# Optimization experiments

Measured on AMD Instinct MI355X. Metric: run time of the kernel, lower is better.

Reference implementation:

```python
import jax, jax.numpy as jnp
import numpy as np

B, N, HID = 2, 1024, 2048
H, KVH, D = 16, 4, 128
GROUPS = H // KVH
FLA_W = 0.5
GATE_NORM = 16.0  # gate_logit_normalizer in source


def setup_inputs() -> dict:
    key = jax.random.key(0)
    ks = jax.random.split(key, 5)
    s = 0.02
    return {
        "hidden_states": jax.random.normal(ks[0], (B, N, HID), jnp.float32),
        "Wq": jax.random.normal(ks[1], (HID, H * D), jnp.float32) * s,
        "Wk": jax.random.normal(ks[2], (HID, KVH * D), jnp.float32) * s,
        "Wv": jax.random.normal(ks[3], (HID, KVH * D), jnp.float32) * s,
        "Wo": jax.random.normal(ks[4], (H * D, HID), jnp.float32) * s,
    }


def _heads(x, h):
    # (B, N, h*D) -> (B, h, N, D)
    return x.reshape(B, N, h, D).transpose(0, 2, 1, 3)


def _repeat_kv(x):
    # (B, KVH, N, D) -> (B, H, N, D), each kv head repeated GROUPS times
    return jnp.repeat(x, GROUPS, axis=1)


def _delta_rule(q, k, v, beta):
    # q,k,v,beta: (L, D). Token-level delta-rule recurrence, mathematically
    # identical to the chunked algorithm for any chunk_size.
    # S_t = S_{t-1} + k_t (beta_t * (v_t - S_{t-1}^T k_t))^T ;  o_t = S_t^T q_t
    Dk = q.shape[-1]
    Dv = v.shape[-1]

    def step(S, inp):
        qi, ki, vi, bi = inp
        u = bi * (vi - ki @ S)          # (Dv,)
        S = S + jnp.outer(ki, u)        # (Dk, Dv)
        return S, qi @ S                # o_t

    S0 = jnp.zeros((Dk, Dv), q.dtype)
    _, o = jax.lax.scan(step, S0, (q, k, v, beta))
    return o


def reference(hidden_states, Wq, Wk, Wv, Wo):
    q = hidden_states @ Wq              # (B, N, H*D)
    k = hidden_states @ Wk              # (B, N, KVH*D)
    v = hidden_states @ Wv              # (B, N, KVH*D)
    g = k  # AdaptiveAvgPool1d(output=KVH*D) over a length-(KVH*D) axis == identity

    qh = _heads(q, H)                   # (B, H, N, D)
    kh = _repeat_kv(_heads(k, KVH))     # (B, H, N, D)
    vh = _repeat_kv(_heads(v, KVH))
    gh = _repeat_kv(_heads(g, KVH))

    # --- linear (delta-rule) branch ---
    ql = jax.nn.softmax(qh, axis=-1)
    kl = jax.nn.softmax(kh, axis=-1)
    gl = jax.nn.log_sigmoid(gh) / GATE_NORM
    # faithful to source: flatten (B,H,N,D) -> (B*H*N, D), single recurrence
    o_lin = _delta_rule(
        ql.reshape(-1, D), kl.reshape(-1, D),
        vh.reshape(-1, D), gl.reshape(-1, D),
    )
    o_lin = o_lin.reshape(B, H, N, D).transpose(0, 2, 1, 3).reshape(B, N, H * D)
    o_lin = o_lin @ Wo                  # (B, N, HID)

    # --- base attention branch (causal GQA softmax attention) ---
    scale = 1.0 / np.sqrt(D).astype(np.float32)
    scores = jnp.einsum('bhnd,bhmd->bhnm', qh, kh) * scale  # (B,H,N,N)
    causal = jnp.tril(jnp.ones((N, N), bool))
    scores = jnp.where(causal, scores, jnp.finfo(scores.dtype).min)
    attn = jax.nn.softmax(scores, axis=-1)
    o_base = jnp.einsum('bhnm,bhmd->bhnd', attn, vh)
    o_base = o_base.transpose(0, 2, 1, 3).reshape(B, N, H * D) @ Wo

    out = FLA_W * o_lin + (1.0 - FLA_W) * o_base
    return out
```

## Files before the change

kernel.cpp:

```cpp
#include <hip/hip_runtime.h>
#include <hip/hip_bf16.h>
#include <hip/hip_fp16.h>
#include <math.h>

#define BB 2
#define NN 1024
#define HID 2048
#define NH 16
#define KVH 4
#define DD 128
#define L_TOTAL 32768
#define TOK 2048
#define NCHUNK 512

typedef __bf16 bf16;
typedef __bf16 bf16x8 __attribute__((ext_vector_type(8)));
typedef __bf16 bf16x4 __attribute__((ext_vector_type(4)));
typedef float f32x4 __attribute__((ext_vector_type(4)));

template<bool SPLIT, bool OUTBF>
__global__ __launch_bounds__(256)
void gemm_bt(const bf16* __restrict__ A, const bf16* __restrict__ Alo,
             const bf16* __restrict__ B, const bf16* __restrict__ Blo,
             float* __restrict__ Cf, bf16* __restrict__ Cb,
             int M, int N, int K, int lda, int ldb, int ldc,
             long aSb, long aSh, long aSz, long bSb, long bSh, long cSz,
             int zH, int gShift, int z0)
{
    const int zc   = blockIdx.z;
    const int z    = zc + z0;
    const int b    = z / zH;
    const int h    = z % zH;
    const int lane = threadIdx.x & 63;
    const int wave = threadIdx.x >> 6;
    const int tiles_n = N >> 4;
    const int tile = blockIdx.x * 4 + wave;
    const int mt   = tile / tiles_n;
    const int nt   = tile % tiles_n;

    const long aoff = (long)b * aSb + (long)h * aSh + (long)zc * aSz;
    const long boff = (long)b * bSb + (long)(h >> gShift) * bSh;

    const bf16* ap = A + aoff + (long)(mt * 16 + (lane & 15)) * lda + ((lane >> 4) << 3);
    const bf16* bp = B + boff + (long)(nt * 16 + (lane & 15)) * ldb + ((lane >> 4) << 3);

    f32x4 acc = {0.f, 0.f, 0.f, 0.f};
    if (!SPLIT) {
        for (int k0 = 0; k0 < K; k0 += 32) {
            bf16x8 av = *(const bf16x8*)ap;
            bf16x8 bv = *(const bf16x8*)bp;
            acc = __builtin_amdgcn_mfma_f32_16x16x32_bf16(av, bv, acc, 0, 0, 0);
            ap += 32; bp += 32;
        }
    } else {
        const bf16* apl = Alo + (ap - A);
        const bf16* bpl = Blo + (bp - B);
        for (int k0 = 0; k0 < K; k0 += 32) {
            bf16x8 av = *(const bf16x8*)ap;
            bf16x8 bv = *(const bf16x8*)bp;
            bf16x8 al = *(const bf16x8*)apl;
            bf16x8 bl = *(const bf16x8*)bpl;
            acc = __builtin_amdgcn_mfma_f32_16x16x32_bf16(av, bv, acc, 0, 0, 0);
            acc = __builtin_amdgcn_mfma_f32_16x16x32_bf16(al, bv, acc, 0, 0, 0);
            acc = __builtin_amdgcn_mfma_f32_16x16x32_bf16(av, bl, acc, 0, 0, 0);
            ap += 32; bp += 32; apl += 32; bpl += 32;
        }
    }

    const long cbase = (long)zc * cSz + (long)(nt * 16 + (lane & 15));
    const int  r0    = mt * 16 + ((lane >> 4) << 2);
    #pragma unroll
    for (int r = 0; r < 4; ++r) {
        long idx = cbase + (long)(r0 + r) * ldc;
        if (OUTBF) Cb[idx] = (bf16)acc[r];
        else       Cf[idx] = acc[r];
    }
}

__global__ void cast_split_k(const float* __restrict__ in, bf16* __restrict__ hi,
                             bf16* __restrict__ lo, long n)
{
    long i = (long)blockIdx.x * blockDim.x + threadIdx.x;
    if (i < n) {
        float x = in[i];
        bf16 h = (bf16)x;
        hi[i] = h;
        lo[i] = (bf16)(x - (float)h);
    }
}

__global__ void cast_k(const float* __restrict__ in, bf16* __restrict__ out, long n)
{
    long i = (long)blockIdx.x * blockDim.x + threadIdx.x;
    if (i < n) out[i] = (bf16)in[i];
}

__global__ void transpose_split_k(const float* __restrict__ in, bf16* __restrict__ hi,
                                  bf16* __restrict__ lo, int K, int N)
{
    long i = (long)blockIdx.x * blockDim.x + threadIdx.x;
    if (i < (long)K * N) {
        int n = (int)(i / K);
        int k = (int)(i % K);
        float x = in[(long)k * N + n];
        bf16 h = (bf16)x;
        hi[i] = h;
        lo[i] = (bf16)(x - (float)h);
    }
}

__global__ void vtrans_k(const float* __restrict__ v, bf16* __restrict__ vT)
{
    long i = (long)blockIdx.x * blockDim.x + threadIdx.x;
    if (i < 1048576) {
        int m   = (int)(i & 1023);
        int d   = (int)((i >> 10) & 127);
        int kvh = (int)((i >> 17) & 3);
        int b   = (int)(i >> 19);
        vT[i] = (bf16)v[((long)(b * 1024 + m)) * 512 + kvh * 128 + d];
    }
}

__global__ void softmax128_k(const float* __restrict__ in, float* __restrict__ out)
{
    const int row  = blockIdx.x;
    const int lane = threadIdx.x;
    float2 v = ((const float2*)(in + (long)row * 128))[lane];
    float m = fmaxf(v.x, v.y);
    #pragma unroll
    for (int s = 1; s < 64; s <<= 1) m = fmaxf(m, __shfl_xor(m, s, 64));
    float ex = expf(v.x - m), ey = expf(v.y - m);
    float sum = ex + ey;
    #pragma unroll
    for (int s = 1; s < 64; s <<= 1) sum += __shfl_xor(sum, s, 64);
    float inv = 1.0f / sum;
    ((float2*)(out + (long)row * 128))[lane] = make_float2(ex * inv, ey * inv);
}

__global__ void logsig_k(const float* __restrict__ in, float* __restrict__ out, long n)
{
    long i = (long)blockIdx.x * blockDim.x + threadIdx.x;
    if (i < n) {
        float x = in[i];
        float l = log1pf(expf(-fabsf(x)));
        out[i] = (fminf(x, 0.f) - l) * 0.0625f;
    }
}

__global__ void softmax_causal_k(bf16* __restrict__ P)
{
    const int row  = blockIdx.x;
    const int qi   = row & 1023;
    const int lane = threadIdx.x;
    bf16* p = P + (long)row * 1024;
    const float scale = 0.08838834764831845f;
    float vals[16];
    float m = -3.0e38f;
    #pragma unroll
    for (int t = 0; t < 16; ++t) {
        int j = lane + t * 64;
        float x = (j <= qi) ? (float)p[j] * scale : -3.0e38f;
        vals[t] = x;
        m = fmaxf(m, x);
    }
    #pragma unroll
    for (int s = 1; s < 64; s <<= 1) m = fmaxf(m, __shfl_xor(m, s, 64));
    float sum = 0.f;
    #pragma unroll
    for (int t = 0; t < 16; ++t) {
        float e = (vals[t] > -1.0e38f) ? expf(vals[t] - m) : 0.f;
        vals[t] = e;
        sum += e;
    }
    #pragma unroll
    for (int s = 1; s < 64; s <<= 1) sum += __shfl_xor(sum, s, 64);
    float inv = 1.f / sum;
    #pragma unroll
    for (int t = 0; t < 16; ++t) {
        int j = lane + t * 64;
        p[j] = (bf16)(vals[t] * inv);
    }
}

__global__ void ktrans_k(const float* __restrict__ KLb, bf16* __restrict__ KThi,
                         bf16* __restrict__ KTlo)
{
    long i = (long)blockIdx.x * blockDim.x + threadIdx.x;
    if (i < 1048576) {
        int t = (int)(i & 63);
        int d = (int)((i >> 6) & 127);
        int a = (int)(i >> 13);
        int b = a >> 6, kvh = (a >> 4) & 3, nc = a & 15;
        float x = KLb[((long)(b * 1024 + nc * 64 + t)) * 512 + kvh * 128 + d];
        bf16 h = (bf16)x;
        KThi[i] = h;
        KTlo[i] = (bf16)(x - (float)h);
    }
}

__global__ __launch_bounds__(256)
void prepA_mfma_k(const bf16* __restrict__ KLhi, const bf16* __restrict__ KLlo,
                  bf16* __restrict__ Abhi, bf16* __restrict__ Ablo,
                  float* __restrict__ ATf)
{
    const int a = blockIdx.x;
    const int b = a >> 6, kvh = (a >> 4) & 3, nc = a & 15;
    const long rbase = ((long)(b * 1024 + nc * 64)) * 512 + kvh * 128;
    const int wave = threadIdx.x >> 6, lane = threadIdx.x & 63;
    const int l15 = lane & 15, kq = lane >> 4;

    #pragma unroll
    for (int it = 0; it < 4; ++it) {
        const int tile = wave * 4 + it;
        const int mt = tile >> 2, nt = tile & 3;
        f32x4 acc = {0.f, 0.f, 0.f, 0.f};
        if (nt <= mt) {
            const long arow = rbase + (long)(mt * 16 + l15) * 512 + kq * 8;
            const long brow = rbase + (long)(nt * 16 + l15) * 512 + kq * 8;
            #pragma unroll
            for (int ki = 0; ki < 4; ++ki) {
                bf16x8 ah = *(const bf16x8*)(KLhi + arow + ki * 32);
                bf16x8 al = *(const bf16x8*)(KLlo + arow + ki * 32);
                bf16x8 bh = *(const bf16x8*)(KLhi + brow + ki * 32);
                bf16x8 bl = *(const bf16x8*)(KLlo + brow + ki * 32);
                acc = __builtin_amdgcn_mfma_f32_16x16x32_bf16(ah, bh, acc, 0, 0, 0);
                acc = __builtin_amdgcn_mfma_f32_16x16x32_bf16(al, bh, acc, 0, 0, 0);
                acc = __builtin_amdgcn_mfma_f32_16x16x32_bf16(ah, bl, acc, 0, 0, 0);
            }
        }
        const int s  = nt * 16 + l15;
        const int r0 = mt * 16 + kq * 4;
        #pragma unroll
        for (int r = 0; r < 4; ++r) {
            int t = r0 + r;
            float dot = (s < t) ? acc[r] : 0.f;
            bf16 hh = (bf16)dot;
            Abhi[(long)a * 4096 + t * 64 + s] = hh;
            Ablo[(long)a * 4096 + t * 64 + s] = (bf16)(dot - (float)hh);
            ATf[(long)a * 4096 + s * 64 + t] = dot;
        }
    }
}

__global__ __launch_bounds__(256)
void prepAq_mfma_k(const bf16* __restrict__ QLhi, const bf16* __restrict__ QLlo,
                   const bf16* __restrict__ KLhi, const bf16* __restrict__ KLlo,
                   bf16* __restrict__ Aqhi, bf16* __restrict__ Aqlo)
{
    const int c = blockIdx.x;
    const int b = c >> 8, h = (c >> 4) & 15, nc = c & 15, kvh = h >> 2;
    const long qb = ((long)(b * 1024 + nc * 64)) * 2048 + h * 128;
    const long kb = ((long)(b * 1024 + nc * 64)) * 512 + kvh * 128;
    const int wave = threadIdx.x >> 6, lane = threadIdx.x & 63;
    const int l15 = lane & 15, kq = lane >> 4;

    #pragma unroll
    for (int it = 0; it < 4; ++it) {
        const int tile = wave * 4 + it;
        const int mt = tile >> 2, nt = tile & 3;
        f32x4 acc = {0.f, 0.f, 0.f, 0.f};
        if (nt <= mt) {
            const long arow = qb + (long)(mt * 16 + l15) * 2048 + kq * 8;
            const long brow = kb + (long)(nt * 16 + l15) * 512 + kq * 8;
            #pragma unroll
            for (int ki = 0; ki < 4; ++ki) {
                bf16x8 ah = *(const bf16x8*)(QLhi + arow + ki * 32);
                bf16x8 al = *(const bf16x8*)(QLlo + arow + ki * 32);
                bf16x8 bh = *(const bf16x8*)(KLhi + brow + ki * 32);
                bf16x8 bl = *(const bf16x8*)(KLlo + brow + ki * 32);
                acc = __builtin_amdgcn_mfma_f32_16x16x32_bf16(ah, bh, acc, 0, 0, 0);
                acc = __builtin_amdgcn_mfma_f32_16x16x32_bf16(al, bh, acc, 0, 0, 0);
                acc = __builtin_amdgcn_mfma_f32_16x16x32_bf16(ah, bl, acc, 0, 0, 0);
            }
        }
        const int s  = nt * 16 + l15;
        const int r0 = mt * 16 + kq * 4;
        #pragma unroll
        for (int r = 0; r < 4; ++r) {
            int t = r0 + r;
            float dot = (s <= t) ? acc[r] : 0.f;
            bf16 hh = (bf16)dot;
            Aqhi[(long)c * 4096 + t * 64 + s] = hh;
            Aqlo[(long)c * 4096 + t * 64 + s] = (bf16)(dot - (float)hh);
        }
    }
}

__global__ __launch_bounds__(64, 1)
void seq_scan_k(const bf16* __restrict__ KLhi, const bf16* __restrict__ KLlo,
                const bf16* __restrict__ KThi, const bf16* __restrict__ KTlo,
                const bf16* __restrict__ Abhi, const bf16* __restrict__ Ablo,
                const float* __restrict__ ATf, const float* __restrict__ vf,
                const float* __restrict__ GLb,
                bf16* __restrict__ S0Thi, bf16* __restrict__ S0Tlo,
                bf16* __restrict__ uTghi, bf16* __restrict__ uTglo)
{
    __shared__ __align__(16) bf16  SThi[16 * 128];
    __shared__ __align__(16) bf16  STlo[16 * 128];
    __shared__ __align__(16) bf16  uThi[16 * 64];
    __shared__ __align__(16) bf16  uTlo[16 * 64];
    __shared__ __align__(16) float xb[64 * 16];
    __shared__ __align__(16) float ATl[4096];

    const int lane  = threadIdx.x;
    const int jloc  = lane & 15;
    const int kq    = lane >> 4;
    const int jglob = blockIdx.x * 16 + jloc;

    for (int i = lane; i < 16 * 128; i += 64) { SThi[i] = (bf16)0.f; STlo[i] = (bf16)0.f; }
    for (int i = lane; i < 16 * 128; i += 64) {
        int j = i >> 7, d = i & 127;
        long off = (long)(blockIdx.x * 16 + j) * 128 + d;
        S0Thi[off] = (bf16)0.f;
        S0Tlo[off] = (bf16)0.f;
    }

    f32x4 S[8];
    #pragma unroll
    for (int m = 0; m < 8; ++m) S[m] = (f32x4){0.f, 0.f, 0.f, 0.f};

    for (int c = 0; c < NCHUNK; ++c) {
        const int b = c >> 8, h = (c >> 4) & 15, nc = c & 15;
        const int kvh = h >> 2, n0 = nc * 64;
        const long krow0  = ((long)(b * 1024 + n0)) * 512 + kvh * 128;
        const int  achunk = (b * 4 + kvh) * 16 + nc;
        const long abase  = (long)achunk * 4096;
        const long ktbase = (long)achunk * 8192;

        bf16x8 klh[16], kll[16];
        #pragma unroll
        for (int m = 0; m < 4; ++m)
            #pragma unroll
            for (int ki = 0; ki < 4; ++ki) {
                long ko = krow0 + (long)(m * 16 + jloc) * 512 + ki * 32 + kq * 8;
                klh[m * 4 + ki] = *(const bf16x8*)(KLhi + ko);
                kll[m * 4 + ki] = *(const bf16x8*)(KLlo + ko);
            }

        float4 atReg[16];
        {
            const float* src = ATf + abase;
            #pragma unroll
            for (int u = 0; u < 16; ++u)
                atReg[u] = *(const float4*)(src + u * 256 + lane * 4);
        }

        bf16x8 abh[4], abl[4];
        #pragma unroll
        for (int q = 0; q < 4; ++q) {
            const int tt = (q < 2) ? (16 + q * 16) : 48;
            const int kk = (q == 3) ? 1 : 0;
            long ao = abase + (long)(tt + jloc) * 64 + kk * 32 + kq * 8;
            abh[q] = *(const bf16x8*)(Abhi + ao);
            abl[q] = *(const bf16x8*)(Ablo + ao);
        }

        float Vv[2][16], Bv[2][16];
        {
            const long vrow0 = ((long)(b * 1024 + n0)) * 512 + kvh * 128 + jglob;
            #pragma unroll
            for (int s = 0; s < 16; ++s) {
                Vv[0][s] = vf[vrow0 + (long)s * 512];
                Bv[0][s] = GLb[vrow0 + (long)s * 512];
            }
        }

        f32x4 W[4];
        #pragma unroll
        for (int m = 0; m < 4; ++m) W[m] = (f32x4){0.f, 0.f, 0.f, 0.f};
        #pragma unroll
        for (int ki = 0; ki < 4; ++ki) {
            bf16x8 sh = *(const bf16x8*)&SThi[jloc * 128 + ki * 32 + kq * 8];
            bf16x8 sl = *(const bf16x8*)&STlo[jloc * 128 + ki * 32 + kq * 8];
            #pragma unroll
            for (int m = 0; m < 4; ++m) {
                W[m] = __builtin_amdgcn_mfma_f32_16x16x32_bf16(klh[m * 4 + ki], sh, W[m], 0, 0, 0);
                W[m] = __builtin_amdgcn_mfma_f32_16x16x32_bf16(kll[m * 4 + ki], sh, W[m], 0, 0, 0);
                W[m] = __builtin_amdgcn_mfma_f32_16x16x32_bf16(klh[m * 4 + ki], sl, W[m], 0, 0, 0);
            }
        }
        #pragma unroll
        for (int m = 0; m < 4; ++m)
            #pragma unroll
            for (int r = 0; r < 4; ++r)
                xb[(m * 16 + kq * 4 + r) * 16 + jloc] = W[m][r];

        #pragma unroll
        for (int u = 0; u < 16; ++u)
            *(float4*)(ATl + u * 256 + lane * 4) = atReg[u];

        bf16x8 kth[16], ktl[16];
        #pragma unroll
        for (int m = 0; m < 8; ++m)
            #pragma unroll
            for (int ki = 0; ki < 2; ++ki) {
                long o = ktbase + (long)(m * 16 + jloc) * 64 + ki * 32 + kq * 8;
                kth[m * 2 + ki] = *(const bf16x8*)(KThi + o);
                ktl[m * 2 + ki] = *(const bf16x8*)(KTlo + o);
            }

        {
            uint4 z = {0u, 0u, 0u, 0u};
            ((uint4*)uThi)[lane] = z; ((uint4*)uThi)[lane + 64] = z;
            ((uint4*)uTlo)[lane] = z; ((uint4*)uTlo)[lane + 64] = z;
        }

        #pragma unroll
        for (int i = 0; i < 4; ++i) {
            const int T0 = i * 16;
            if (i > 0) {
                const int K32 = (i + 1) >> 1;
                const int fb  = i - 1;
                f32x4 corr = (f32x4){0.f, 0.f, 0.f, 0.f};
                #pragma unroll
                for (int ki = 0; ki < 2; ++ki) if (ki < K32) {
                    bf16x8 uh = *(const bf16x8*)&uThi[jloc * 64 + ki * 32 + kq * 8];
                    bf16x8 ul = *(const bf16x8*)&uTlo[jloc * 64 + ki * 32 + kq * 8];
                    corr = __builtin_amdgcn_mfma_f32_16x16x32_bf16(uh, abh[fb + ki], corr, 0, 0, 0);
                    corr = __builtin_amdgcn_mfma_f32_16x16x32_bf16(ul, abh[fb + ki], corr, 0, 0, 0);
                    corr = __builtin_amdgcn_mfma_f32_16x16x32_bf16(uh, abl[fb + ki], corr, 0, 0, 0);
                }
                #pragma unroll
                for (int r = 0; r < 4; ++r)
                    xb[(T0 + jloc) * 16 + kq * 4 + r] += corr[r];
            }

            float Xv[16];
            #pragma unroll
            for (int s = 0; s < 16; ++s) Xv[s] = xb[(T0 + s) * 16 + jloc];

            if (i < 3) {
                const long vrow0n = ((long)(b * 1024 + n0 + T0 + 16)) * 512 + kvh * 128 + jglob;
                #pragma unroll
                for (int s = 0; s < 16; ++s) {
                    Vv[(i + 1) & 1][s] = vf[vrow0n + (long)s * 512];
                    Bv[(i + 1) & 1][s] = GLb[vrow0n + (long)s * 512];
                }
            }

            float rb[4][16];
            #pragma unroll
            for (int p = 0; p < 4; ++p) {
                const float* rp = ATl + (T0 + p) * 64 + T0;
                #pragma unroll
                for (int g = 0; g < 4; ++g) {
                    float4 v4 = *(const float4*)(rp + g * 4);
                    rb[p][g * 4 + 0] = v4.x; rb[p][g * 4 + 1] = v4.y;
                    rb[p][g * 4 + 2] = v4.z; rb[p][g * 4 + 3] = v4.w;
                }
            }

            float acc[16];
            #pragma unroll
            for (int t = 0; t < 16; ++t) acc[t] = 0.f;

            #pragma unroll
            for (int s = 0; s < 16; ++s) {
                float u = Bv[i & 1][s] * (Vv[i & 1][s] - Xv[s] - acc[s]);
                bf16 uh = (bf16)u;
                bf16 ul = (bf16)(u - (float)uh);
                if (lane < 16) {
                    uThi[jloc * 64 + T0 + s] = uh;
                    uTlo[jloc * 64 + T0 + s] = ul;
                }
                #pragma unroll
                for (int t = 0; t < 16; ++t)
                    if (t > s) acc[t] += rb[s & 3][t] * u;
                {
                    int rr = T0 + s + 4; if (rr > 63) rr = 63;
                    const float* rp = ATl + rr * 64 + T0;
                    #pragma unroll
                    for (int g = 0; g < 4; ++g) {
                        float4 v4 = *(const float4*)(rp + g * 4);
                        rb[s & 3][g * 4 + 0] = v4.x; rb[s & 3][g * 4 + 1] = v4.y;
                        rb[s & 3][g * 4 + 2] = v4.z; rb[s & 3][g * 4 + 3] = v4.w;
                    }
                }
            }
        }

        #pragma unroll
        for (int ki = 0; ki < 2; ++ki) {
            bf16x8 uh = *(const bf16x8*)&uThi[jloc * 64 + ki * 32 + kq * 8];
            bf16x8 ul = *(const bf16x8*)&uTlo[jloc * 64 + ki * 32 + kq * 8];
            #pragma unroll
            for (int m = 0; m < 8; ++m) {
                S[m] = __builtin_amdgcn_mfma_f32_16x16x32_bf16(kth[m * 2 + ki], uh, S[m], 0, 0, 0);
                S[m] = __builtin_amdgcn_mfma_f32_16x16x32_bf16(kth[m * 2 + ki], ul, S[m], 0, 0, 0);
                S[m] = __builtin_amdgcn_mfma_f32_16x16x32_bf16(ktl[m * 2 + ki], uh, S[m], 0, 0, 0);
            }
        }

        {
            const uint4* uh4 = (const uint4*)uThi;
            const uint4* ul4 = (const uint4*)uTlo;
            uint4* gh = (uint4*)(uTghi + ((long)c * 128 + blockIdx.x * 16) * 64);
            uint4* gl = (uint4*)(uTglo + ((long)c * 128 + blockIdx.x * 16) * 64);
            gh[lane] = uh4[lane]; gh[lane + 64] = uh4[lane + 64];
            gl[lane] = ul4[lane]; gl[lane + 64] = ul4[lane + 64];
        }

        #pragma unroll
        for (int m = 0; m < 8; ++m) {
            bf16x4 h4, l4;
            #pragma unroll
            for (int r = 0; r < 4; ++r) {
                float v = S[m][r];
                bf16 hh = (bf16)v;
                h4[r] = hh;
                l4[r] = (bf16)(v - (float)hh);
            }
            int d0 = m * 16 + kq * 4;
            *(bf16x4*)&SThi[jloc * 128 + d0] = h4;
            *(bf16x4*)&STlo[jloc * 128 + d0] = l4;
            long goff = (long)(c + 1) * 16384 + (long)jglob * 128 + d0;
            *(bf16x4*)(S0Thi + goff) = h4;
            *(bf16x4*)(S0Tlo + goff) = l4;
        }
    }
}

__global__ __launch_bounds__(256)
void pass2_o_k(const bf16* __restrict__ QLhi, const bf16* __restrict__ QLlo,
               const bf16* __restrict__ S0Thi, const bf16* __restrict__ S0Tlo,
               const bf16* __restrict__ Aqhi, const bf16* __restrict__ Aqlo,
               const bf16* __restrict__ uTghi, const bf16* __restrict__ uTglo,
               float* __restrict__ O)
{
    const int c    = blockIdx.x >> 3;
    const int tg   = blockIdx.x & 7;
    const int wave = threadIdx.x >> 6;
    const int lane = threadIdx.x & 63;
    const int tt   = tg * 4 + wave;
    const int mt   = tt >> 3, nt = tt & 7;
    const int b = c >> 8, h = (c >> 4) & 15, nc = c & 15, n0 = nc * 64;
    const int kq = lane >> 4, l15 = lane & 15;

    const long qrow   = ((long)(b * 1024 + n0 + mt * 16 + l15)) * 2048 + h * 128;
    const long sbase  = (long)c * 16384 + (long)(nt * 16 + l15) * 128;
    const long aqbase = (long)c * 4096 + (long)(mt * 16 + l15) * 64;
    const long ubase  = ((long)(c * 128 + nt * 16 + l15)) * 64;

    f32x4 acc = {0.f, 0.f, 0.f, 0.f};
    #pragma unroll
    for (int ki = 0; ki < 4; ++ki) {
        bf16x8 qh = *(const bf16x8*)(QLhi + qrow + ki * 32 + kq * 8);
        bf16x8 ql = *(const bf16x8*)(QLlo + qrow + ki * 32 + kq * 8);
        bf16x8 sh = *(const bf16x8*)(S0Thi + sbase + ki * 32 + kq * 8);
        bf16x8 sl = *(const bf16x8*)(S0Tlo + sbase + ki * 32 + kq * 8);
        acc = __builtin_amdgcn_mfma_f32_16x16x32_bf16(qh, sh, acc, 0, 0, 0);
        acc = __builtin_amdgcn_mfma_f32_16x16x32_bf16(ql, sh, acc, 0, 0, 0);
        acc = __builtin_amdgcn_mfma_f32_16x16x32_bf16(qh, sl, acc, 0, 0, 0);
    }
    #pragma unroll
    for (int ki = 0; ki < 2; ++ki) {
        bf16x8 ah = *(const bf16x8*)(Aqhi + aqbase + ki * 32 + kq * 8);
        bf16x8 al = *(const bf16x8*)(Aqlo + aqbase + ki * 32 + kq * 8);
        bf16x8 uh = *(const bf16x8*)(uTghi + ubase + ki * 32 + kq * 8);
        bf16x8 ul = *(const bf16x8*)(uTglo + ubase + ki * 32 + kq * 8);
        acc = __builtin_amdgcn_mfma_f32_16x16x32_bf16(ah, uh, acc, 0, 0, 0);
        acc = __builtin_amdgcn_mfma_f32_16x16x32_bf16(al, uh, acc, 0, 0, 0);
        acc = __builtin_amdgcn_mfma_f32_16x16x32_bf16(ah, ul, acc, 0, 0, 0);
    }
    #pragma unroll
    for (int r = 0; r < 4; ++r)
        O[((long)c * 64 + mt * 16 + kq * 4 + r) * 128 + nt * 16 + l15] = acc[r];
}

__global__ void combine_k(const float* __restrict__ oLin, const bf16* __restrict__ oBase,
                          bf16* __restrict__ oComb, long n)
{
    long i = (long)blockIdx.x * blockDim.x + threadIdx.x;
    if (i < n) {
        int d  = (int)(i & 127);
        int hh = (int)((i >> 7) & 15);
        int nn = (int)((i >> 11) & 1023);
        int b  = (int)(i >> 21);
        long src = ((long)((b * 16 + hh) * 1024 + nn)) * 128 + d;
        oComb[i] = (bf16)(0.5f * (oLin[src] + (float)oBase[src]));
    }
}

extern "C" void kernel_launch(void* const* d_in, const int* in_sizes, int n_in,
                              void* d_out, int out_size, void* d_ws, size_t ws_size,
                              hipStream_t stream)
{
    const float* hs = (const float*)d_in[0];
    const float* Wq = (const float*)d_in[1];
    const float* Wk = (const float*)d_in[2];
    const float* Wv = (const float*)d_in[3];
    const float* Wo = (const float*)d_in[4];

    char* base = (char*)d_ws;
    size_t off = 0;
    auto alloc = [&](size_t bytes) -> char* {
        char* r = base + off;
        off += (bytes + 255) & ~(size_t)255;
        return r;
    };

    bf16* hsHi  = (bf16*)alloc((long)TOK * 2048 * 2);
    bf16* hsLo  = (bf16*)alloc((long)TOK * 2048 * 2);
    bf16* WqTHi = (bf16*)alloc(2048L * 2048 * 2);
    bf16* WqTLo = (bf16*)alloc(2048L * 2048 * 2);
    bf16* WkTHi = (bf16*)alloc(512L * 2048 * 2);
    bf16* WkTLo = (bf16*)alloc(512L * 2048 * 2);
    bf16* WvTHi = (bf16*)alloc(512L * 2048 * 2);
    bf16* WvTLo = (bf16*)alloc(512L * 2048 * 2);
    bf16* WoTHi = (bf16*)alloc(2048L * 2048 * 2);
    bf16* WoTLo = (bf16*)alloc(2048L * 2048 * 2);
    float* qf   = (float*)alloc((long)TOK * 2048 * 4);
    float* kf   = (float*)alloc((long)TOK * 512 * 4);
    float* vf   = (float*)alloc((long)TOK * 512 * 4);
    float* QLb  = (float*)alloc((long)TOK * 2048 * 4);
    float* KLb  = (float*)alloc((long)TOK * 512 * 4);
    float* GLb  = (float*)alloc((long)TOK * 512 * 4);
    bf16* qhB   = (bf16*)alloc((long)TOK * 2048 * 2);
    bf16* khB   = (bf16*)alloc((long)TOK * 512 * 2);
    bf16* vT    = (bf16*)alloc(1048576L * 2);
    bf16* P     = (bf16*)alloc(8L * 1024 * 1024 * 2);
    float* oLin = (float*)alloc(32768L * 128 * 4);
    bf16* oBase = (bf16*)alloc(32768L * 128 * 2);
    bf16* oComb = (bf16*)alloc((long)TOK * 2048 * 2);
    bf16* KLhi  = (bf16*)alloc((long)TOK * 512 * 2);
    bf16* KLlo  = (bf16*)alloc((long)TOK * 512 * 2);
    bf16* QLhi  = (bf16*)alloc((long)TOK * 2048 * 2);
    bf16* QLlo  = (bf16*)alloc((long)TOK * 2048 * 2);
    bf16* KThi  = (bf16*)alloc(1048576L * 2);
    bf16* KTlo  = (bf16*)alloc(1048576L * 2);
    bf16* Abhi  = (bf16*)alloc(128L * 4096 * 2);
    bf16* Ablo  = (bf16*)alloc(128L * 4096 * 2);
    float* ATf  = (float*)alloc(128L * 4096 * 4);
    bf16* Aqhi  = (bf16*)alloc(512L * 4096 * 2);
    bf16* Aqlo  = (bf16*)alloc(512L * 4096 * 2);
    bf16* S0Thi = (bf16*)alloc(513L * 16384 * 2);
    bf16* S0Tlo = (bf16*)alloc(513L * 16384 * 2);
    bf16* uTghi = (bf16*)alloc(512L * 128 * 64 * 2);
    bf16* uTglo = (bf16*)alloc(512L * 128 * 64 * 2);

    const int T256 = 256;
    cast_split_k<<<(TOK * 2048 + 255) / 256, T256, 0, stream>>>(hs, hsHi, hsLo, (long)TOK * 2048);
    transpose_split_k<<<(2048L * 2048 + 255) / 256, T256, 0, stream>>>(Wq, WqTHi, WqTLo, 2048, 2048);
    transpose_split_k<<<(2048L * 512 + 255) / 256, T256, 0, stream>>>(Wk, WkTHi, WkTLo, 2048, 512);
    transpose_split_k<<<(2048L * 512 + 255) / 256, T256, 0, stream>>>(Wv, WvTHi, WvTLo, 2048, 512);
    transpose_split_k<<<(2048L * 2048 + 255) / 256, T256, 0, stream>>>(Wo, WoTHi, WoTLo, 2048, 2048);

    gemm_bt<true, false><<<dim3(4096, 1, 1), T256, 0, stream>>>(
        hsHi, hsLo, WqTHi, WqTLo, qf, nullptr,
        2048, 2048, 2048, 2048, 2048, 2048, 0, 0, 0, 0, 0, 0, 1, 0, 0);
    gemm_bt<true, false><<<dim3(1024, 1, 1), T256, 0, stream>>>(
        hsHi, hsLo, WkTHi, WkTLo, kf, nullptr,
        2048, 512, 2048, 2048, 2048, 512, 0, 0, 0, 0, 0, 0, 1, 0, 0);
    gemm_bt<true, false><<<dim3(1024, 1, 1), T256, 0, stream>>>(
        hsHi, hsLo, WvTHi, WvTLo, vf, nullptr,
        2048, 512, 2048, 2048, 2048, 512, 0, 0, 0, 0, 0, 0, 1, 0, 0);

    softmax128_k<<<32768, 64, 0, stream>>>(qf, QLb);
    softmax128_k<<<8192, 64, 0, stream>>>(kf, KLb);
    logsig_k<<<(1048576 + 255) / 256, T256, 0, stream>>>(kf, GLb, 1048576);

    cast_k<<<(TOK * 2048 + 255) / 256, T256, 0, stream>>>(qf, qhB, (long)TOK * 2048);
    cast_k<<<(TOK * 512 + 255) / 256, T256, 0, stream>>>(kf, khB, (long)TOK * 512);
    vtrans_k<<<(1048576 + 255) / 256, T256, 0, stream>>>(vf, vT);

    cast_split_k<<<(TOK * 512 + 255) / 256, T256, 0, stream>>>(KLb, KLhi, KLlo, (long)TOK * 512);
    cast_split_k<<<(TOK * 2048 + 255) / 256, T256, 0, stream>>>(QLb, QLhi, QLlo, (long)TOK * 2048);
    ktrans_k<<<(1048576 + 255) / 256, T256, 0, stream>>>(KLb, KThi, KTlo);
    prepA_mfma_k<<<128, T256, 0, stream>>>(KLhi, KLlo, Abhi, Ablo, ATf);
    prepAq_mfma_k<<<512, T256, 0, stream>>>(QLhi, QLlo, KLhi, KLlo, Aqhi, Aqlo);

    for (int z0 = 0; z0 < 32; z0 += 8) {
        gemm_bt<false, true><<<dim3(1024, 1, 8), T256, 0, stream>>>(
            qhB, nullptr, khB, nullptr, nullptr, P,
            1024, 1024, 128, 2048, 512, 1024,
            2097152L, 128L, 0L, 524288L, 128L, 1048576L, 16, 2, z0);
        softmax_causal_k<<<8192, 64, 0, stream>>>(P);
        gemm_bt<false, true><<<dim3(128, 1, 8), T256, 0, stream>>>(
            P, nullptr, vT, nullptr, nullptr, oBase + (long)z0 * 131072,
            1024, 128, 1024, 1024, 1024, 128,
            0L, 0L, 1048576L, 524288L, 131072L, 131072L, 16, 2, z0);
    }

    seq_scan_k<<<8, 64, 0, stream>>>(KLhi, KLlo, KThi, KTlo, Abhi, Ablo, ATf, vf, GLb,
                                     S0Thi, S0Tlo, uTghi, uTglo);
    pass2_o_k<<<4096, T256, 0, stream>>>(QLhi, QLlo, S0Thi, S0Tlo, Aqhi, Aqlo,
                                         uTghi, uTglo, oLin);

    combine_k<<<(TOK * 2048 + 255) / 256, T256, 0, stream>>>(oLin, oBase, oComb, (long)TOK * 2048);
    gemm_bt<false, false><<<dim3(4096, 1, 1), T256, 0, stream>>>(
        oComb, nullptr, WoTHi, nullptr, (float*)d_out, nullptr,
        2048, 2048, 2048, 2048, 2048, 2048, 0, 0, 0, 0, 0, 0, 1, 0, 0);
}
```

Measured before the change: 5.469 ms.

## Register-block GEMM into 64x64 per-wave tiles with 128x128 block tiles

The bf16 MFMA GEMM is changed from one 16x16 output tile per wave to a 4x4 grid of 16x16 tiles per wave (64x64), with four waves forming a 128x128 block tile. Each loaded A and B fragment is now reused across four MFMAs, cutting redundant global loads that the old kernel spent on every output tile. All GEMM launches shrink their grids to match. In exchange it needs many more accumulator registers per wave, which may lower occupancy, and the small P@V GEMMs now launch only a few blocks, which may underfill the GPU.

```diff
diff --git a/kernel.cpp b/kernel.cpp
--- a/kernel.cpp
+++ b/kernel.cpp
@@ -20,12 +20,12 @@
 
 template<bool SPLIT, bool OUTBF>
 __global__ __launch_bounds__(256)
-void gemm_bt(const bf16* __restrict__ A, const bf16* __restrict__ Alo,
-             const bf16* __restrict__ B, const bf16* __restrict__ Blo,
-             float* __restrict__ Cf, bf16* __restrict__ Cb,
-             int M, int N, int K, int lda, int ldb, int ldc,
-             long aSb, long aSh, long aSz, long bSb, long bSh, long cSz,
-             int zH, int gShift, int z0)
+void gemm64_bt(const bf16* __restrict__ A, const bf16* __restrict__ Alo,
+               const bf16* __restrict__ B, const bf16* __restrict__ Blo,
+               float* __restrict__ Cf, bf16* __restrict__ Cb,
+               int M, int N, int K, int lda, int ldb, int ldc,
+               long aSb, long aSh, long aSz, long bSb, long bSh, long cSz,
+               int zH, int gShift, int z0)
 {
     const int zc   = blockIdx.z;
     const int z    = zc + z0;
@@ -33,48 +33,74 @@
     const int h    = z % zH;
     const int lane = threadIdx.x & 63;
     const int wave = threadIdx.x >> 6;
-    const int tiles_n = N >> 4;
-    const int tile = blockIdx.x * 4 + wave;
-    const int mt   = tile / tiles_n;
-    const int nt   = tile % tiles_n;
+    const int tiles_n = N >> 7;
+    const int btm = blockIdx.x / tiles_n;
+    const int btn = blockIdx.x % tiles_n;
+    const int wr = wave >> 1, wc = wave & 1;
+    const int r0 = btm * 128 + wr * 64;
+    const int c0 = btn * 128 + wc * 64;
+    const int l15 = lane & 15, kq = lane >> 4;
 
     const long aoff = (long)b * aSb + (long)h * aSh + (long)zc * aSz;
     const long boff = (long)b * bSb + (long)(h >> gShift) * bSh;
 
-    const bf16* ap = A + aoff + (long)(mt * 16 + (lane & 15)) * lda + ((lane >> 4) << 3);
-    const bf16* bp = B + boff + (long)(nt * 16 + (lane & 15)) * ldb + ((lane >> 4) << 3);
-
-    f32x4 acc = {0.f, 0.f, 0.f, 0.f};
-    if (!SPLIT) {
-        for (int k0 = 0; k0 < K; k0 += 32) {
-            bf16x8 av = *(const bf16x8*)ap;
-            bf16x8 bv = *(const bf16x8*)bp;
-            acc = __builtin_amdgcn_mfma_f32_16x16x32_bf16(av, bv, acc, 0, 0, 0);
-            ap += 32; bp += 32;
-        }
-    } else {
-        const bf16* apl = Alo + (ap - A);
-        const bf16* bpl = Blo + (bp - B);
-        for (int k0 = 0; k0 < K; k0 += 32) {
-            bf16x8 av = *(const bf16x8*)ap;
-            bf16x8 bv = *(const bf16x8*)bp;
-            bf16x8 al = *(const bf16x8*)apl;
-            bf16x8 bl = *(const bf16x8*)bpl;
-            acc = __builtin_amdgcn_mfma_f32_16x16x32_bf16(av, bv, acc, 0, 0, 0);
-            acc = __builtin_amdgcn_mfma_f32_16x16x32_bf16(al, bv, acc, 0, 0, 0);
-            acc = __builtin_amdgcn_mfma_f32_16x16x32_bf16(av, bl, acc, 0, 0, 0);
-            ap += 32; bp += 32; apl += 32; bpl += 32;
-        }
-    }
-
-    const long cbase = (long)zc * cSz + (long)(nt * 16 + (lane & 15));
-    const int  r0    = mt * 16 + ((lane >> 4) << 2);
-    #pragma unroll
-    for (int r = 0; r < 4; ++r) {
-        long idx = cbase + (long)(r0 + r) * ldc;
-        if (OUTBF) Cb[idx] = (bf16)acc[r];
-        else       Cf[idx] = acc[r];
-    }
+    const bf16* ap[4];
+    const bf16* bp[4];
+    #pragma unroll
+    for (int m = 0; m < 4; ++m)
+        ap[m] = A + aoff + (long)(r0 + m * 16 + l15) * lda + kq * 8;
+    #pragma unroll
+    for (int n = 0; n < 4; ++n)
+        bp[n] = B + boff + (long)(c0 + n * 16 + l15) * ldb + kq * 8;
+
+    f32x4 acc[4][4];
+    #pragma unroll
+    for (int m = 0; m < 4; ++m)
+        #pragma unroll
+        for (int n = 0; n < 4; ++n)
+            acc[m][n] = (f32x4){0.f, 0.f, 0.f, 0.f};
+
+    for (int k0 = 0; k0 < K; k0 += 32) {
+        bf16x8 ah[4], bh[4], al[4], bl[4];
+        #pragma unroll
+        for (int m = 0; m < 4; ++m) {
+            ah[m] = *(const bf16x8*)ap[m];
+            if (SPLIT) al[m] = *(const bf16x8*)(Alo + (ap[m] - A));
+        }
+        #pragma unroll
+        for (int n = 0; n < 4; ++n) {
+            bh[n] = *(const bf16x8*)bp[n];
+            if (SPLIT) bl[n] = *(const bf16x8*)(Blo + (bp[n] - B));
+        }
+        #pragma unroll
+        for (int m = 0; m < 4; ++m)
+            #pragma unroll
+            for (int n = 0; n < 4; ++n) {
+                acc[m][n] = __builtin_amdgcn_mfma_f32_16x16x32_bf16(ah[m], bh[n], acc[m][n], 0, 0, 0);
+                if (SPLIT) {
+                    acc[m][n] = __builtin_amdgcn_mfma_f32_16x16x32_bf16(al[m], bh[n], acc[m][n], 0, 0, 0);
+                    acc[m][n] = __builtin_amdgcn_mfma_f32_16x16x32_bf16(ah[m], bl[n], acc[m][n], 0, 0, 0);
+                }
+            }
+        #pragma unroll
+        for (int m = 0; m < 4; ++m) ap[m] += 32;
+        #pragma unroll
+        for (int n = 0; n < 4; ++n) bp[n] += 32;
+    }
+
+    #pragma unroll
+    for (int m = 0; m < 4; ++m)
+        #pragma unroll
+        for (int n = 0; n < 4; ++n) {
+            const long cbase = (long)zc * cSz + (long)(c0 + n * 16 + l15);
+            const int  rr0   = r0 + m * 16 + kq * 4;
+            #pragma unroll
+            for (int r = 0; r < 4; ++r) {
+                long idx = cbase + (long)(rr0 + r) * ldc;
+                if (OUTBF) Cb[idx] = (bf16)acc[m][n][r];
+                else       Cf[idx] = acc[m][n][r];
+            }
+        }
 }
 
 __global__ void cast_split_k(const float* __restrict__ in, bf16* __restrict__ hi,
@@ -645,13 +671,13 @@
     transpose_split_k<<<(2048L * 512 + 255) / 256, T256, 0, stream>>>(Wv, WvTHi, WvTLo, 2048, 512);
     transpose_split_k<<<(2048L * 2048 + 255) / 256, T256, 0, stream>>>(Wo, WoTHi, WoTLo, 2048, 2048);
 
-    gemm_bt<true, false><<<dim3(4096, 1, 1), T256, 0, stream>>>(
+    gemm64_bt<true, false><<<dim3(256, 1, 1), T256, 0, stream>>>(
         hsHi, hsLo, WqTHi, WqTLo, qf, nullptr,
         2048, 2048, 2048, 2048, 2048, 2048, 0, 0, 0, 0, 0, 0, 1, 0, 0);
-    gemm_bt<true, false><<<dim3(1024, 1, 1), T256, 0, stream>>>(
+    gemm64_bt<true, false><<<dim3(64, 1, 1), T256, 0, stream>>>(
         hsHi, hsLo, WkTHi, WkTLo, kf, nullptr,
         2048, 512, 2048, 2048, 2048, 512, 0, 0, 0, 0, 0, 0, 1, 0, 0);
-    gemm_bt<true, false><<<dim3(1024, 1, 1), T256, 0, stream>>>(
+    gemm64_bt<true, false><<<dim3(64, 1, 1), T256, 0, stream>>>(
         hsHi, hsLo, WvTHi, WvTLo, vf, nullptr,
         2048, 512, 2048, 2048, 2048, 512, 0, 0, 0, 0, 0, 0, 1, 0, 0);
 
@@ -670,12 +696,12 @@
     prepAq_mfma_k<<<512, T256, 0, stream>>>(QLhi, QLlo, KLhi, KLlo, Aqhi, Aqlo);
 
     for (int z0 = 0; z0 < 32; z0 += 8) {
-        gemm_bt<false, true><<<dim3(1024, 1, 8), T256, 0, stream>>>(
+        gemm64_bt<false, true><<<dim3(64, 1, 8), T256, 0, stream>>>(
             qhB, nullptr, khB, nullptr, nullptr, P,
             1024, 1024, 128, 2048, 512, 1024,
             2097152L, 128L, 0L, 524288L, 128L, 1048576L, 16, 2, z0);
         softmax_causal_k<<<8192, 64, 0, stream>>>(P);
-        gemm_bt<false, true><<<dim3(128, 1, 8), T256, 0, stream>>>(
+        gemm64_bt<false, true><<<dim3(8, 1, 8), T256, 0, stream>>>(
             P, nullptr, vT, nullptr, nullptr, oBase + (long)z0 * 131072,
             1024, 128, 1024, 1024, 1024, 128,
             0L, 0L, 1048576L, 524288L, 131072L, 131072L, 16, 2, z0);
@@ -687,7 +713,7 @@
                                          uTghi, uTglo, oLin);
 
     combine_k<<<(TOK * 2048 + 255) / 256, T256, 0, stream>>>(oLin, oBase, oComb, (long)TOK * 2048);
-    gemm_bt<false, false><<<dim3(4096, 1, 1), T256, 0, stream>>>(
+    gemm64_bt<false, false><<<dim3(256, 1, 1), T256, 0, stream>>>(
         oComb, nullptr, WoTHi, nullptr, (float*)d_out, nullptr,
         2048, 2048, 2048, 2048, 2048, 2048, 0, 0, 0, 0, 0, 0, 1, 0, 0);
 }
```

Result: faster. 4.896 ms (-10.5%).
